# Kernel optimization log

Hardware: AMD Instinct MI355X
Metric: run time of the kernel (lower is better)

## Reference

```python
import jax, jax.numpy as jnp
import numpy as np


def setup_inputs() -> dict:
    key = jax.random.key(0)
    k1, k2 = jax.random.split(key)
    B, C, H, W = 32, 256, 64, 64
    data = jax.random.normal(k1, (B, C, H, W), dtype=jnp.float32)
    offset = jax.random.normal(k2, (B, 2, H, W), dtype=jnp.float32)
    trans_std = jnp.float32(0.005)  # learned scalar Parameter
    return {"data": data, "offset": offset, "trans_std": trans_std}


def reference(data, offset, trans_std):
    """Offset-driven bilinear interpolation sampling + global average pooling.

    data:   [B, C, H, W]
    offset: [B, 2, H, W]  (dy, dx) displacement field, scaled by trans_std
    Returns pooled features [B, C].
    """
    B, C, H, W = data.shape
    ts = jnp.clip(trans_std, 0.001, 0.01)  # forward clamps trans_std to [0.001, 0.01]

    # sampling coordinates: base grid + scaled offsets (offsets normalized by H/W)
    ii = jnp.arange(H, dtype=data.dtype)[:, None]   # [H,1]
    jj = jnp.arange(W, dtype=data.dtype)[None, :]   # [1,W]
    y = jnp.clip(ii + ts * offset[:, 0] * H, 0.0, H - 1)  # [B,H,W]
    x = jnp.clip(jj + ts * offset[:, 1] * W, 0.0, W - 1)  # [B,H,W]

    y0 = jnp.clip(jnp.floor(y).astype(jnp.int32), 0, H - 2)
    x0 = jnp.clip(jnp.floor(x).astype(jnp.int32), 0, W - 2)
    y1 = y0 + 1
    x1 = x0 + 1
    wy = y - y0.astype(data.dtype)  # [B,H,W] in [0,1]
    wx = x - x0.astype(data.dtype)

    def sample_one(d, yy0, yy1, xx0, xx1):
        # d: [C,H,W]; index maps: [H,W] -> gathered [C,H,W]
        v00 = d[:, yy0, xx0]
        v01 = d[:, yy0, xx1]
        v10 = d[:, yy1, xx0]
        v11 = d[:, yy1, xx1]
        return v00, v01, v10, v11

    v00, v01, v10, v11 = jax.vmap(sample_one)(data, y0, y1, x0, x1)  # each [B,C,H,W]

    wy_ = wy[:, None]  # broadcast over channels -> [B,1,H,W]
    wx_ = wx[:, None]
    sampled = ((1 - wy_) * (1 - wx_) * v00 + (1 - wy_) * wx_ * v01
               + wy_ * (1 - wx_) * v10 + wy_ * wx_ * v11)  # [B,C,H,W]

    # pooling: global average over spatial locations -> [B,C]
    return jnp.mean(sampled, axis=(2, 3))
```

## Files before the change

### kernel.cpp

```cpp
#include <hip/hip_runtime.h>

#define BATCH 32
#define CHAN  256
#define HGT   64
#define WID   64
#define HW    4096

__global__ __launch_bounds__(256) void weight_map_kernel(
        const float* __restrict__ offset,
        const float* __restrict__ ts_ptr,
        float* __restrict__ A)
{
    const int b   = blockIdx.x;
    const int tid = threadIdx.x;

    __shared__ float acc[HW];
    for (int k = tid; k < HW; k += 256) acc[k] = 0.0f;
    __syncthreads();

    float ts = ts_ptr[0];
    ts = fminf(fmaxf(ts, 0.001f), 0.01f);

    const float* off_y = offset + (size_t)b * 2 * HW;
    const float* off_x = off_y + HW;

    for (int p = tid; p < HW; p += 256) {
        const int i = p >> 6;
        const int j = p & 63;
        const float dy = off_y[p];
        const float dx = off_x[p];
        float y = fminf(fmaxf((float)i + ts * dy * 64.0f, 0.0f), 63.0f);
        float x = fminf(fmaxf((float)j + ts * dx * 64.0f, 0.0f), 63.0f);
        int y0 = (int)floorf(y); y0 = min(max(y0, 0), HGT - 2);
        int x0 = (int)floorf(x); x0 = min(max(x0, 0), WID - 2);
        const float wy = y - (float)y0;
        const float wx = x - (float)x0;
        const int base = (y0 << 6) + x0;
        atomicAdd(&acc[base],           (1.0f - wy) * (1.0f - wx));
        atomicAdd(&acc[base + 1],       (1.0f - wy) * wx);
        atomicAdd(&acc[base + WID],     wy * (1.0f - wx));
        atomicAdd(&acc[base + WID + 1], wy * wx);
    }
    __syncthreads();

    float* Ab = A + (size_t)b * HW;
    const float s = 1.0f / (float)HW;
    for (int k = tid; k < HW; k += 256) Ab[k] = acc[k] * s;
}

__global__ __launch_bounds__(256) void dot_kernel(
        const float* __restrict__ data,
        const float* __restrict__ A,
        float* __restrict__ out)
{
    const int blk = blockIdx.x;
    const int b   = blk >> 8;
    const int tid = threadIdx.x;

    const float* plane = data + (size_t)blk * HW;
    const float* Ab    = A    + (size_t)b   * HW;

    float sum = 0.0f;
    #pragma unroll
    for (int it = 0; it < 4; ++it) {
        const int idx = (it * 256 + tid) * 4;
        const float4 dv = *reinterpret_cast<const float4*>(plane + idx);
        const float4 av = *reinterpret_cast<const float4*>(Ab + idx);
        sum = fmaf(av.x, dv.x, sum);
        sum = fmaf(av.y, dv.y, sum);
        sum = fmaf(av.z, dv.z, sum);
        sum = fmaf(av.w, dv.w, sum);
    }

    #pragma unroll
    for (int off = 32; off > 0; off >>= 1)
        sum += __shfl_down(sum, off, 64);

    __shared__ float wsum[4];
    const int lane = tid & 63;
    const int wv   = tid >> 6;
    if (lane == 0) wsum[wv] = sum;
    __syncthreads();
    if (tid == 0) {
        out[blk] = wsum[0] + wsum[1] + wsum[2] + wsum[3];
    }
}

extern "C" void kernel_launch(void* const* d_in, const int* in_sizes, int n_in,
                              void* d_out, int out_size, void* d_ws, size_t ws_size,
                              hipStream_t stream) {
    const float* data   = (const float*)d_in[0];
    const float* offset = (const float*)d_in[1];
    const float* ts     = (const float*)d_in[2];

    float* A   = (float*)d_ws;
    float* out = (float*)d_out;

    weight_map_kernel<<<BATCH, 256, 0, stream>>>(offset, ts, A);
    dot_kernel<<<BATCH * CHAN, 256, 0, stream>>>(data, A, out);
}
```

Baseline: 209.7 us.

## Fuse weight-map scatter and channel dot product into a single kernel

Merges the two kernels into one. Each block rebuilds the per-batch bilinear weight map in shared memory, then dots it against 16 channels held in registers. This removes the global round trip of the weight map and one launch, and lets the serial 32-block weight-map stage spread across 512 blocks. In exchange, every block repeats the offset scatter, so that work is done 16 times per batch. Occupancy drops to fewer, larger blocks with a 16-wide register accumulator.

```diff
diff --git a/kernel.cpp b/kernel.cpp
--- a/kernel.cpp
+++ b/kernel.cpp
@@ -5,17 +5,25 @@
 #define HGT   64
 #define WID   64
 #define HW    4096
+#define BPB   16
+#define CPB   (CHAN / BPB)
 
-__global__ __launch_bounds__(256) void weight_map_kernel(
+__global__ __launch_bounds__(256, 2) void fused_bilinear_pool(
+        const float* __restrict__ data,
         const float* __restrict__ offset,
         const float* __restrict__ ts_ptr,
-        float* __restrict__ A)
+        float* __restrict__ out)
 {
-    const int b   = blockIdx.x;
+    const int blk = blockIdx.x;
+    const int b   = blk >> 4;
+    const int c0  = (blk & (BPB - 1)) * CPB;
     const int tid = threadIdx.x;
 
     __shared__ float acc[HW];
-    for (int k = tid; k < HW; k += 256) acc[k] = 0.0f;
+    __shared__ float wred[4][CPB];
+
+    #pragma unroll
+    for (int it = 0; it < 16; ++it) acc[it * 256 + tid] = 0.0f;
     __syncthreads();
 
     float ts = ts_ptr[0];
@@ -24,65 +32,68 @@
     const float* off_y = offset + (size_t)b * 2 * HW;
     const float* off_x = off_y + HW;
 
-    for (int p = tid; p < HW; p += 256) {
-        const int i = p >> 6;
-        const int j = p & 63;
-        const float dy = off_y[p];
-        const float dx = off_x[p];
-        float y = fminf(fmaxf((float)i + ts * dy * 64.0f, 0.0f), 63.0f);
-        float x = fminf(fmaxf((float)j + ts * dx * 64.0f, 0.0f), 63.0f);
-        int y0 = (int)floorf(y); y0 = min(max(y0, 0), HGT - 2);
-        int x0 = (int)floorf(x); x0 = min(max(x0, 0), WID - 2);
-        const float wy = y - (float)y0;
-        const float wx = x - (float)x0;
-        const int base = (y0 << 6) + x0;
-        atomicAdd(&acc[base],           (1.0f - wy) * (1.0f - wx));
-        atomicAdd(&acc[base + 1],       (1.0f - wy) * wx);
-        atomicAdd(&acc[base + WID],     wy * (1.0f - wx));
-        atomicAdd(&acc[base + WID + 1], wy * wx);
+    #pragma unroll
+    for (int it = 0; it < 4; ++it) {
+        const int p4 = (it * 256 + tid) * 4;
+        const float4 dy4 = *reinterpret_cast<const float4*>(off_y + p4);
+        const float4 dx4 = *reinterpret_cast<const float4*>(off_x + p4);
+        const int i  = p4 >> 6;
+        const int j0 = p4 & 63;
+        const float dys[4] = {dy4.x, dy4.y, dy4.z, dy4.w};
+        const float dxs[4] = {dx4.x, dx4.y, dx4.z, dx4.w};
+        #pragma unroll
+        for (int e = 0; e < 4; ++e) {
+            float y = fminf(fmaxf((float)i + ts * dys[e] * 64.0f, 0.0f), 63.0f);
+            float x = fminf(fmaxf((float)(j0 + e) + ts * dxs[e] * 64.0f, 0.0f), 63.0f);
+            int y0 = (int)floorf(y); y0 = min(max(y0, 0), HGT - 2);
+            int x0 = (int)floorf(x); x0 = min(max(x0, 0), WID - 2);
+            const float wy = y - (float)y0;
+            const float wx = x - (float)x0;
+            const int base = (y0 << 6) + x0;
+            atomicAdd(&acc[base],           (1.0f - wy) * (1.0f - wx));
+            atomicAdd(&acc[base + 1],       (1.0f - wy) * wx);
+            atomicAdd(&acc[base + WID],     wy * (1.0f - wx));
+            atomicAdd(&acc[base + WID + 1], wy * wx);
+        }
     }
     __syncthreads();
 
-    float* Ab = A + (size_t)b * HW;
-    const float s = 1.0f / (float)HW;
-    for (int k = tid; k < HW; k += 256) Ab[k] = acc[k] * s;
-}
+    float sums[CPB];
+    #pragma unroll
+    for (int ci = 0; ci < CPB; ++ci) sums[ci] = 0.0f;
 
-__global__ __launch_bounds__(256) void dot_kernel(
-        const float* __restrict__ data,
-        const float* __restrict__ A,
-        float* __restrict__ out)
-{
-    const int blk = blockIdx.x;
-    const int b   = blk >> 8;
-    const int tid = threadIdx.x;
+    const float* plane0 = data + ((size_t)b * CHAN + c0) * HW;
 
-    const float* plane = data + (size_t)blk * HW;
-    const float* Ab    = A    + (size_t)b   * HW;
-
-    float sum = 0.0f;
     #pragma unroll
     for (int it = 0; it < 4; ++it) {
         const int idx = (it * 256 + tid) * 4;
-        const float4 dv = *reinterpret_cast<const float4*>(plane + idx);
-        const float4 av = *reinterpret_cast<const float4*>(Ab + idx);
-        sum = fmaf(av.x, dv.x, sum);
-        sum = fmaf(av.y, dv.y, sum);
-        sum = fmaf(av.z, dv.z, sum);
-        sum = fmaf(av.w, dv.w, sum);
+        const float4 av = *reinterpret_cast<const float4*>(acc + idx);
+        #pragma unroll
+        for (int ci = 0; ci < CPB; ++ci) {
+            const float4 dv =
+                *reinterpret_cast<const float4*>(plane0 + (size_t)ci * HW + idx);
+            sums[ci] = fmaf(av.x, dv.x, sums[ci]);
+            sums[ci] = fmaf(av.y, dv.y, sums[ci]);
+            sums[ci] = fmaf(av.z, dv.z, sums[ci]);
+            sums[ci] = fmaf(av.w, dv.w, sums[ci]);
+        }
     }
 
-    #pragma unroll
-    for (int off = 32; off > 0; off >>= 1)
-        sum += __shfl_down(sum, off, 64);
-
-    __shared__ float wsum[4];
     const int lane = tid & 63;
     const int wv   = tid >> 6;
-    if (lane == 0) wsum[wv] = sum;
+    #pragma unroll
+    for (int ci = 0; ci < CPB; ++ci) {
+        float v = sums[ci];
+        #pragma unroll
+        for (int off = 32; off > 0; off >>= 1)
+            v += __shfl_down(v, off, 64);
+        if (lane == 0) wred[wv][ci] = v;
+    }
     __syncthreads();
-    if (tid == 0) {
-        out[blk] = wsum[0] + wsum[1] + wsum[2] + wsum[3];
+
+    if (tid < CPB) {
+        const float r = wred[0][tid] + wred[1][tid] + wred[2][tid] + wred[3][tid];
+        out[(b << 8) + c0 + tid] = r * (1.0f / (float)HW);
     }
 }
 
@@ -93,9 +104,8 @@
     const float* offset = (const float*)d_in[1];
     const float* ts     = (const float*)d_in[2];
 
-    float* A   = (float*)d_ws;
     float* out = (float*)d_out;
+    (void)d_ws; (void)ws_size;
 
-    weight_map_kernel<<<BATCH, 256, 0, stream>>>(offset, ts, A);
-    dot_kernel<<<BATCH * CHAN, 256, 0, stream>>>(data, A, out);
+    fused_bilinear_pool<<<BATCH * BPB, 256, 0, stream>>>(data, offset, ts, out);
 }
```

New measurement: 220.5 us. 5.2% more time.
